# Kernel optimization log

Measured on AMD Instinct MI355X. Metric: run time of the kernel, lower is better.

Reference implementation:

```python
import jax, jax.numpy as jnp
import numpy as np

B, H, S, D = 4, 16, 2048, 128

def setup_inputs() -> dict:
    key = jax.random.key(0)
    kq, kk, kv = jax.random.split(key, 3)
    Q = jax.random.normal(kq, (B, H, S, D), dtype=jnp.float32)
    K = jax.random.normal(kk, (B, H, S, D), dtype=jnp.float32)
    V = jax.random.normal(kv, (B, H, S, D), dtype=jnp.float32)
    # causal mask: True = attend (lower triangle incl. diagonal)
    mask = jnp.tril(jnp.ones((S, S), dtype=jnp.bool_))[None, None, :, :]
    return {"Q": Q, "K": K, "V": V, "mask": mask}

def reference(Q, K, V, mask):
    d_k = Q.shape[-1]
    scale = 1.0 / jnp.sqrt(jnp.asarray(d_k, Q.dtype))
    # [B,H,Sq,Sk] score matrix (naive, materialized, as in the original)
    scores = jnp.einsum('bhqd,bhkd->bhqk', Q, K) * scale
    scores = jnp.where(mask, scores, jnp.asarray(-1e9, scores.dtype))
    attn = jax.nn.softmax(scores, axis=-1)
    return jnp.einsum('bhqk,bhkd->bhqd', attn, V)
```

## Files before the change

kernel.cpp:

```cpp
#include <hip/hip_runtime.h>
#include <hip/hip_bf16.h>

constexpr int S_LEN = 2048;
constexpr int D_DIM = 128;
constexpr int NBH   = 64;
constexpr int NKT   = 32;
constexpr size_t TILE_SHORTS = 64 * 128;
constexpr size_t PAIR_SHORTS = 2 * TILE_SHORTS;
constexpr size_t WS_NEEDED   = (size_t)NBH * NKT * PAIR_SHORTS * 2;

typedef __attribute__((ext_vector_type(8))) short short8;
typedef __attribute__((ext_vector_type(4))) float f32x4;

__device__ __forceinline__ short f2bf(float f) {
    unsigned u = __builtin_bit_cast(unsigned, f);
    u += 0x7fffu + ((u >> 16) & 1u);
    return (short)(u >> 16);
}

__device__ __forceinline__ int kpos(int dc, int key) { return dc ^ (key & 15); }
__device__ __forceinline__ int vpos(int kc, int d) {
    return kc ^ ((d >> 3) & 7) ^ (d & 7);
}

__global__ __launch_bounds__(256)
void preprocess_kv(const float* __restrict__ K, const float* __restrict__ V,
                   short* __restrict__ ws) {
    __shared__ short sv[128 * 64];
    const int tid = threadIdx.x;
    const int kt  = blockIdx.x;
    const int bh  = blockIdx.y;
    const size_t inbase = ((size_t)bh * S_LEN + (size_t)kt * 64) * D_DIM;
    short* wk = ws + ((size_t)bh * NKT + kt) * PAIR_SHORTS;
    short* wv = wk + TILE_SHORTS;

    for (int it = 0; it < 4; ++it) {
        const int idx = (it * 256 + tid) * 8;
        const int key = idx >> 7, d = idx & 127;
        const float* kp = K + inbase + (size_t)key * D_DIM + d;
        float4 a = *reinterpret_cast<const float4*>(kp);
        float4 b = *reinterpret_cast<const float4*>(kp + 4);
        short8 f;
        f[0]=f2bf(a.x); f[1]=f2bf(a.y); f[2]=f2bf(a.z); f[3]=f2bf(a.w);
        f[4]=f2bf(b.x); f[5]=f2bf(b.y); f[6]=f2bf(b.z); f[7]=f2bf(b.w);
        *reinterpret_cast<short8*>(&wk[key * 128 + (kpos(d >> 3, key) << 3)]) = f;
        const float* vp = V + inbase + (size_t)key * D_DIM + d;
        float4 c = *reinterpret_cast<const float4*>(vp);
        float4 e = *reinterpret_cast<const float4*>(vp + 4);
        float vals[8] = {c.x,c.y,c.z,c.w,e.x,e.y,e.z,e.w};
        for (int j = 0; j < 8; ++j) {
            const int dr = d + j;
            sv[dr * 64 + (vpos(key >> 3, dr) << 3) + (key & 7)] = f2bf(vals[j]);
        }
    }
    __syncthreads();
    for (int it = 0; it < 4; ++it) {
        const int off = (it * 256 + tid) * 8;
        *reinterpret_cast<short8*>(&wv[off]) =
            *reinterpret_cast<const short8*>(&sv[off]);
    }
}

__device__ __forceinline__ void async_copy_1k(const short* gsrc, short* ldst,
                                              int lane) {
    __builtin_amdgcn_global_load_lds(
        (const __attribute__((address_space(1))) void*)(gsrc + lane * 8),
        (__attribute__((address_space(3))) void*)ldst, 16, 0, 0);
}

__global__ __launch_bounds__(512, 4)
void fa_causal_main(const float* __restrict__ Q, const short* __restrict__ ws,
                    float* __restrict__ Out) {
    __shared__ short sK[2][64 * 128];
    __shared__ short sVt[128 * 64];
    __shared__ short sP [128 * 64];

    const int tid  = threadIdx.x;
    const int wid  = tid >> 6;
    const int lane = tid & 63;
    const int quad = lane >> 4;
    const int l16  = lane & 15;

    const int k_ = blockIdx.x;
    const int j_ = blockIdx.y;
    const int bh = k_ * 8 + (j_ >> 3);
    const int x  = j_ & 7;

    const size_t base = (size_t)bh * S_LEN * D_DIM;
    const short* tiles = ws + (size_t)bh * NKT * PAIR_SHORTS;
    const float qscale = 0.08838834764831845f * 1.44269504088896340f;

    int nb = 0;
    for (int pi = 0; pi < 2; ++pi) {
        const int qt = (pi == 0) ? (15 - x) : x;
        const int q0 = qt * 128;
        const int kend = 2 * qt + 2;

        for (int i = 0; i < 2; ++i) {
            const int s = wid * 2 + i;
            async_copy_1k(tiles + s * 512, &sK[nb][s * 512], lane);
        }
        short8 vr0, vr1;
        {
            const short* vp = tiles + TILE_SHORTS;
            vr0 = *reinterpret_cast<const short8*>(vp + tid * 8);
            vr1 = *reinterpret_cast<const short8*>(vp + tid * 8 + 4096);
        }

        short8 q_frag[4];
        {
            const float* qp = Q + base + (size_t)(q0 + wid * 16 + l16) * D_DIM;
            for (int kk = 0; kk < 4; ++kk) {
                const int d0 = kk * 32 + quad * 8;
                float4 a = *reinterpret_cast<const float4*>(qp + d0);
                float4 b = *reinterpret_cast<const float4*>(qp + d0 + 4);
                short8 f;
                f[0]=f2bf(a.x*qscale); f[1]=f2bf(a.y*qscale);
                f[2]=f2bf(a.z*qscale); f[3]=f2bf(a.w*qscale);
                f[4]=f2bf(b.x*qscale); f[5]=f2bf(b.y*qscale);
                f[6]=f2bf(b.z*qscale); f[7]=f2bf(b.w*qscale);
                q_frag[kk] = f;
            }
        }

        f32x4 o_acc[8];
        for (int i = 0; i < 8; ++i) o_acc[i] = f32x4{0.f,0.f,0.f,0.f};
        float m_i[4], l_i[4];
        for (int r = 0; r < 4; ++r) { m_i[r] = -1e30f; l_i[r] = 0.f; }

        for (int kt = 0; kt < kend; ++kt) {
            __syncthreads();

            *reinterpret_cast<short8*>(&sVt[tid * 8]) = vr0;
            *reinterpret_cast<short8*>(&sVt[tid * 8 + 4096]) = vr1;

            if (kt + 1 < kend) {
                const short* nk = tiles + (size_t)(kt + 1) * PAIR_SHORTS;
                for (int i = 0; i < 2; ++i) {
                    const int s = wid * 2 + i;
                    async_copy_1k(nk + s * 512, &sK[nb ^ 1][s * 512], lane);
                }
                const short* nv = nk + TILE_SHORTS;
                vr0 = *reinterpret_cast<const short8*>(nv + tid * 8);
                vr1 = *reinterpret_cast<const short8*>(nv + tid * 8 + 4096);
            }

            const int kb    = kt * 64;
            const int wrow0 = q0 + wid * 16;
            const bool active = (kb <= wrow0 + 15);

            f32x4 s_acc[4];
            if (active) {
                __builtin_amdgcn_s_setprio(1);
                for (int ct = 0; ct < 4; ++ct) {
                    const int key = ct * 16 + l16;
                    f32x4 acc = f32x4{0.f,0.f,0.f,0.f};
                    for (int kk = 0; kk < 4; ++kk) {
                        short8 kf = *reinterpret_cast<const short8*>(
                            &sK[nb][key * 128 + (kpos(kk * 4 + quad, key) << 3)]);
                        acc = __builtin_amdgcn_mfma_f32_16x16x32_bf16(q_frag[kk], kf, acc, 0, 0, 0);
                    }
                    s_acc[ct] = acc;
                }
                __builtin_amdgcn_s_setprio(0);

                if (kb + 63 > wrow0) {
                    for (int ct = 0; ct < 4; ++ct) {
                        const int kg = kb + ct * 16 + l16;
                        for (int r = 0; r < 4; ++r)
                            if (kg > wrow0 + quad * 4 + r) s_acc[ct][r] = -1e30f;
                    }
                }

                float tm[4];
                for (int r = 0; r < 4; ++r)
                    tm[r] = fmaxf(fmaxf(s_acc[0][r], s_acc[1][r]),
                                  fmaxf(s_acc[2][r], s_acc[3][r]));
                for (int off = 1; off < 16; off <<= 1)
                    for (int r = 0; r < 4; ++r)
                        tm[r] = fmaxf(tm[r], __shfl_xor(tm[r], off));
                bool grow = false;
                for (int r = 0; r < 4; ++r)
                    grow = grow || (tm[r] - m_i[r] > 8.0f);
                if (__any(grow)) {
                    for (int r = 0; r < 4; ++r) {
                        const float mn = fmaxf(m_i[r], tm[r]);
                        const float a  = __builtin_amdgcn_exp2f(m_i[r] - mn);
                        m_i[r] = mn;
                        l_i[r] *= a;
                        for (int nt = 0; nt < 8; ++nt) o_acc[nt][r] *= a;
                    }
                }
                float rs[4] = {0.f, 0.f, 0.f, 0.f};
                for (int ct = 0; ct < 4; ++ct)
                    for (int r = 0; r < 4; ++r) {
                        const float p = __builtin_amdgcn_exp2f(s_acc[ct][r] - m_i[r]);
                        s_acc[ct][r] = p;
                        rs[r] += p;
                    }
                for (int off = 1; off < 16; off <<= 1)
                    for (int r = 0; r < 4; ++r)
                        rs[r] += __shfl_xor(rs[r], off);
                for (int r = 0; r < 4; ++r) l_i[r] += rs[r];

                for (int ct = 0; ct < 4; ++ct)
                    for (int r = 0; r < 4; ++r) {
                        const int row = wid * 16 + quad * 4 + r;
                        const int col = ct * 16 + l16;
                        sP[row * 64 + (((col >> 3) ^ (row & 7)) << 3) + (col & 7)]
                            = f2bf(s_acc[ct][r]);
                    }
            }

            asm volatile("s_waitcnt lgkmcnt(0)" ::: "memory");
            __builtin_amdgcn_s_barrier();
            asm volatile("" ::: "memory");

            if (active) {
                const int prow = wid * 16 + l16;
                short8 pf[2];
                for (int k2 = 0; k2 < 2; ++k2)
                    pf[k2] = *reinterpret_cast<const short8*>(
                        &sP[prow * 64 + (((k2 * 4 + quad) ^ (prow & 7)) << 3)]);
                __builtin_amdgcn_s_setprio(1);
                for (int nt = 0; nt < 8; ++nt) {
                    const int vrow = nt * 16 + l16;
                    for (int k2 = 0; k2 < 2; ++k2) {
                        short8 vf = *reinterpret_cast<const short8*>(
                            &sVt[vrow * 64 + (vpos(k2 * 4 + quad, vrow) << 3)]);
                        o_acc[nt] = __builtin_amdgcn_mfma_f32_16x16x32_bf16(pf[k2], vf, o_acc[nt], 0, 0, 0);
                    }
                }
                __builtin_amdgcn_s_setprio(0);
            }
            nb ^= 1;
        }

        for (int r = 0; r < 4; ++r) {
            const float inv = 1.0f / l_i[r];
            const int qrow = q0 + wid * 16 + quad * 4 + r;
            float* op = Out + base + (size_t)qrow * D_DIM;
            for (int nt = 0; nt < 8; ++nt)
                op[nt * 16 + l16] = o_acc[nt][r] * inv;
        }
    }
}

constexpr int SK_STRIDE  = 136;
constexpr int SVT_STRIDE = 72;
constexpr int SP_STRIDE  = 72;

__global__ __launch_bounds__(256, 4)
void fa_causal_fallback(const float* __restrict__ Q, const float* __restrict__ K,
                        const float* __restrict__ V, float* __restrict__ Out) {
    __shared__ short sK[64 * SK_STRIDE];
    __shared__ short sVt[128 * SVT_STRIDE];
    short* sP = sK;
    const int tid  = threadIdx.x;
    const int wid  = tid >> 6;
    const int lane = tid & 63;
    const int quad = lane >> 4;
    const int l16  = lane & 15;
    const int x  = blockIdx.x;
    const int bh = blockIdx.y;
    const size_t base = (size_t)bh * S_LEN * D_DIM;
    const float scale = 0.08838834764831845f;
    for (int pi = 0; pi < 2; ++pi) {
        const int qt = (pi == 0) ? (31 - x) : x;
        const int q0 = qt * 64;
        short8 q_frag[4];
        {
            const float* qp = Q + base + (size_t)(q0 + wid * 16 + l16) * D_DIM;
            for (int kk = 0; kk < 4; ++kk) {
                const int d0 = kk * 32 + quad * 8;
                float4 a = *reinterpret_cast<const float4*>(qp + d0);
                float4 b = *reinterpret_cast<const float4*>(qp + d0 + 4);
                short8 f;
                f[0]=f2bf(a.x*scale); f[1]=f2bf(a.y*scale);
                f[2]=f2bf(a.z*scale); f[3]=f2bf(a.w*scale);
                f[4]=f2bf(b.x*scale); f[5]=f2bf(b.y*scale);
                f[6]=f2bf(b.z*scale); f[7]=f2bf(b.w*scale);
                q_frag[kk] = f;
            }
        }
        f32x4 o_acc[8];
        for (int i = 0; i < 8; ++i) o_acc[i] = f32x4{0.f,0.f,0.f,0.f};
        float m_i[4], l_i[4];
        for (int r = 0; r < 4; ++r) { m_i[r] = -1e30f; l_i[r] = 0.f; }
        for (int kt = 0; kt <= qt; ++kt) {
            for (int it = 0; it < 4; ++it) {
                const int idx = (it * 256 + tid) * 8;
                const int key = idx >> 7, d = idx & 127;
                const float* kp = K + base + (size_t)(kt * 64 + key) * D_DIM + d;
                float4 a = *reinterpret_cast<const float4*>(kp);
                float4 b = *reinterpret_cast<const float4*>(kp + 4);
                short8 f;
                f[0]=f2bf(a.x); f[1]=f2bf(a.y); f[2]=f2bf(a.z); f[3]=f2bf(a.w);
                f[4]=f2bf(b.x); f[5]=f2bf(b.y); f[6]=f2bf(b.z); f[7]=f2bf(b.w);
                *reinterpret_cast<short8*>(&sK[key * SK_STRIDE + d]) = f;
            }
            for (int it = 0; it < 4; ++it) {
                const int idx = (it * 256 + tid) * 8;
                const int key = idx >> 7, d = idx & 127;
                const int kc = key >> 3, kw = key & 7;
                const float* vp = V + base + (size_t)(kt * 64 + key) * D_DIM + d;
                float4 a = *reinterpret_cast<const float4*>(vp);
                float4 b = *reinterpret_cast<const float4*>(vp + 4);
                float vals[8] = {a.x,a.y,a.z,a.w,b.x,b.y,b.z,b.w};
                const int rc = (d >> 3) & 7;
                const int cs = (kc ^ rc) * 8 + kw;
                for (int j = 0; j < 8; ++j)
                    sVt[(d + j) * SVT_STRIDE + cs] = f2bf(vals[j]);
            }
            __syncthreads();
            f32x4 s_acc[4];
            for (int ct = 0; ct < 4; ++ct) {
                f32x4 acc = f32x4{0.f,0.f,0.f,0.f};
                for (int kk = 0; kk < 4; ++kk) {
                    short8 kf = *reinterpret_cast<const short8*>(
                        &sK[(ct * 16 + l16) * SK_STRIDE + kk * 32 + quad * 8]);
                    acc = __builtin_amdgcn_mfma_f32_16x16x32_bf16(q_frag[kk], kf, acc, 0, 0, 0);
                }
                s_acc[ct] = acc;
            }
            if (kt == qt) {
                for (int ct = 0; ct < 4; ++ct) {
                    const int kg = ct * 16 + l16;
                    for (int r = 0; r < 4; ++r)
                        if (kg > wid * 16 + quad * 4 + r) s_acc[ct][r] = -1e30f;
                }
            }
            float tm[4];
            for (int r = 0; r < 4; ++r)
                tm[r] = fmaxf(fmaxf(s_acc[0][r], s_acc[1][r]),
                              fmaxf(s_acc[2][r], s_acc[3][r]));
            for (int off = 1; off < 16; off <<= 1)
                for (int r = 0; r < 4; ++r)
                    tm[r] = fmaxf(tm[r], __shfl_xor(tm[r], off));
            float alpha[4], m_new[4], rs[4];
            for (int r = 0; r < 4; ++r) {
                m_new[r] = fmaxf(m_i[r], tm[r]);
                alpha[r] = __expf(m_i[r] - m_new[r]);
                rs[r] = 0.f;
            }
            for (int ct = 0; ct < 4; ++ct)
                for (int r = 0; r < 4; ++r) {
                    float p = __expf(s_acc[ct][r] - m_new[r]);
                    s_acc[ct][r] = p;
                    rs[r] += p;
                }
            for (int off = 1; off < 16; off <<= 1)
                for (int r = 0; r < 4; ++r)
                    rs[r] += __shfl_xor(rs[r], off);
            for (int r = 0; r < 4; ++r) {
                l_i[r] = alpha[r] * l_i[r] + rs[r];
                m_i[r] = m_new[r];
            }
            for (int nt = 0; nt < 8; ++nt)
                for (int r = 0; r < 4; ++r)
                    o_acc[nt][r] *= alpha[r];
            __syncthreads();
            for (int ct = 0; ct < 4; ++ct)
                for (int r = 0; r < 4; ++r) {
                    const int row = wid * 16 + quad * 4 + r;
                    const int col = ct * 16 + l16;
                    sP[row * SP_STRIDE + (((col >> 3) ^ ((row >> 2) & 7)) << 3) + (col & 7)]
                        = f2bf(s_acc[ct][r]);
                }
            {
                const int prow = wid * 16 + l16;
                const int pxr  = (prow >> 2) & 7;
                for (int nt = 0; nt < 8; ++nt) {
                    const int vrow = nt * 16 + l16;
                    const int vxr  = (vrow >> 3) & 7;
                    for (int k2 = 0; k2 < 2; ++k2) {
                        const int chunk = k2 * 4 + quad;
                        short8 pf = *reinterpret_cast<const short8*>(
                            &sP[prow * SP_STRIDE + ((chunk ^ pxr) << 3)]);
                        short8 vf = *reinterpret_cast<const short8*>(
                            &sVt[vrow * SVT_STRIDE + ((chunk ^ vxr) << 3)]);
                        o_acc[nt] = __builtin_amdgcn_mfma_f32_16x16x32_bf16(pf, vf, o_acc[nt], 0, 0, 0);
                    }
                }
            }
            __syncthreads();
        }
        for (int nt = 0; nt < 8; ++nt)
            for (int r = 0; r < 4; ++r) {
                const int qrow = q0 + wid * 16 + quad * 4 + r;
                Out[base + (size_t)qrow * D_DIM + nt * 16 + l16] = o_acc[nt][r] / l_i[r];
            }
    }
}

extern "C" void kernel_launch(void* const* d_in, const int* in_sizes, int n_in,
                              void* d_out, int out_size, void* d_ws, size_t ws_size,
                              hipStream_t stream) {
    const float* Q = (const float*)d_in[0];
    const float* K = (const float*)d_in[1];
    const float* V = (const float*)d_in[2];
    float* Out = (float*)d_out;

    if (ws_size >= WS_NEEDED) {
        short* ws = (short*)d_ws;
        preprocess_kv<<<dim3(NKT, NBH), 256, 0, stream>>>(K, V, ws);
        fa_causal_main<<<dim3(8, NBH), 512, 0, stream>>>(Q, ws, Out);
    } else {
        fa_causal_fallback<<<dim3(16, NBH), 256, 0, stream>>>(Q, K, V, Out);
    }
}
```

Measured before the change: 465.8 us.

## Shrink causal attention blocks to 64-row Q tiles with single-buffered K

Each main-kernel block now owns 64 query rows and runs 4 warps (256 threads) instead of 128 rows and 8 warps. The grid doubles, and a flattened block index is remapped so that batch-head pairs are interleaved. The K tile becomes single-buffered: the next K/V prefetch is issued after the score barrier, and the P-tile store moves after that barrier. Per-warp inactive-tile checks disappear because every warp in a 64-row tile covers the same key range. The aim is to cut causal idle work and LDS footprint and to raise occupancy, at the cost of less K reuse per block and less overlap between loads and compute.

```diff
diff --git a/kernel.cpp b/kernel.cpp
--- a/kernel.cpp
+++ b/kernel.cpp
@@ -68,12 +68,12 @@
         (__attribute__((address_space(3))) void*)ldst, 16, 0, 0);
 }
 
-__global__ __launch_bounds__(512, 4)
+__global__ __launch_bounds__(256, 4)
 void fa_causal_main(const float* __restrict__ Q, const short* __restrict__ ws,
                     float* __restrict__ Out) {
-    __shared__ short sK[2][64 * 128];
+    __shared__ short sK [64 * 128];
     __shared__ short sVt[128 * 64];
-    __shared__ short sP [128 * 64];
+    __shared__ short sP [64 * 64];
 
     const int tid  = threadIdx.x;
     const int wid  = tid >> 6;
@@ -81,30 +81,27 @@
     const int quad = lane >> 4;
     const int l16  = lane & 15;
 
-    const int k_ = blockIdx.x;
-    const int j_ = blockIdx.y;
-    const int bh = k_ * 8 + (j_ >> 3);
-    const int x  = j_ & 7;
+    const int flat = blockIdx.x + (blockIdx.y << 4);
+    const int bh   = ((flat & 7) << 3) | ((flat >> 3) & 7);
+    const int x    = flat >> 6;
 
     const size_t base = (size_t)bh * S_LEN * D_DIM;
     const short* tiles = ws + (size_t)bh * NKT * PAIR_SHORTS;
     const float qscale = 0.08838834764831845f * 1.44269504088896340f;
 
-    int nb = 0;
     for (int pi = 0; pi < 2; ++pi) {
-        const int qt = (pi == 0) ? (15 - x) : x;
-        const int q0 = qt * 128;
-        const int kend = 2 * qt + 2;
-
-        for (int i = 0; i < 2; ++i) {
-            const int s = wid * 2 + i;
-            async_copy_1k(tiles + s * 512, &sK[nb][s * 512], lane);
-        }
-        short8 vr0, vr1;
+        const int qt = (pi == 0) ? (31 - x) : x;
+        const int q0 = qt * 64;
+
+        for (int i = 0; i < 4; ++i) {
+            const int s = wid * 4 + i;
+            async_copy_1k(tiles + s * 512, &sK[s * 512], lane);
+        }
+        short8 vr[4];
         {
             const short* vp = tiles + TILE_SHORTS;
-            vr0 = *reinterpret_cast<const short8*>(vp + tid * 8);
-            vr1 = *reinterpret_cast<const short8*>(vp + tid * 8 + 4096);
+            for (int i = 0; i < 4; ++i)
+                vr[i] = *reinterpret_cast<const short8*>(vp + (i * 256 + tid) * 8);
         }
 
         short8 q_frag[4];
@@ -128,95 +125,89 @@
         float m_i[4], l_i[4];
         for (int r = 0; r < 4; ++r) { m_i[r] = -1e30f; l_i[r] = 0.f; }
 
-        for (int kt = 0; kt < kend; ++kt) {
+        for (int kt = 0; kt <= qt; ++kt) {
             __syncthreads();
 
-            *reinterpret_cast<short8*>(&sVt[tid * 8]) = vr0;
-            *reinterpret_cast<short8*>(&sVt[tid * 8 + 4096]) = vr1;
-
-            if (kt + 1 < kend) {
-                const short* nk = tiles + (size_t)(kt + 1) * PAIR_SHORTS;
-                for (int i = 0; i < 2; ++i) {
-                    const int s = wid * 2 + i;
-                    async_copy_1k(nk + s * 512, &sK[nb ^ 1][s * 512], lane);
-                }
-                const short* nv = nk + TILE_SHORTS;
-                vr0 = *reinterpret_cast<const short8*>(nv + tid * 8);
-                vr1 = *reinterpret_cast<const short8*>(nv + tid * 8 + 4096);
-            }
-
-            const int kb    = kt * 64;
-            const int wrow0 = q0 + wid * 16;
-            const bool active = (kb <= wrow0 + 15);
+            for (int i = 0; i < 4; ++i)
+                *reinterpret_cast<short8*>(&sVt[(i * 256 + tid) * 8]) = vr[i];
 
             f32x4 s_acc[4];
-            if (active) {
-                __builtin_amdgcn_s_setprio(1);
+            __builtin_amdgcn_s_setprio(1);
+            for (int ct = 0; ct < 4; ++ct) {
+                const int key = ct * 16 + l16;
+                f32x4 acc = f32x4{0.f,0.f,0.f,0.f};
+                for (int kk = 0; kk < 4; ++kk) {
+                    short8 kf = *reinterpret_cast<const short8*>(
+                        &sK[key * 128 + (kpos(kk * 4 + quad, key) << 3)]);
+                    acc = __builtin_amdgcn_mfma_f32_16x16x32_bf16(q_frag[kk], kf, acc, 0, 0, 0);
+                }
+                s_acc[ct] = acc;
+            }
+            __builtin_amdgcn_s_setprio(0);
+
+            if (kt == qt) {
                 for (int ct = 0; ct < 4; ++ct) {
-                    const int key = ct * 16 + l16;
-                    f32x4 acc = f32x4{0.f,0.f,0.f,0.f};
-                    for (int kk = 0; kk < 4; ++kk) {
-                        short8 kf = *reinterpret_cast<const short8*>(
-                            &sK[nb][key * 128 + (kpos(kk * 4 + quad, key) << 3)]);
-                        acc = __builtin_amdgcn_mfma_f32_16x16x32_bf16(q_frag[kk], kf, acc, 0, 0, 0);
-                    }
-                    s_acc[ct] = acc;
-                }
-                __builtin_amdgcn_s_setprio(0);
-
-                if (kb + 63 > wrow0) {
-                    for (int ct = 0; ct < 4; ++ct) {
-                        const int kg = kb + ct * 16 + l16;
-                        for (int r = 0; r < 4; ++r)
-                            if (kg > wrow0 + quad * 4 + r) s_acc[ct][r] = -1e30f;
-                    }
-                }
-
-                float tm[4];
+                    const int kg = ct * 16 + l16;
+                    for (int r = 0; r < 4; ++r)
+                        if (kg > wid * 16 + quad * 4 + r) s_acc[ct][r] = -1e30f;
+                }
+            }
+
+            float tm[4];
+            for (int r = 0; r < 4; ++r)
+                tm[r] = fmaxf(fmaxf(s_acc[0][r], s_acc[1][r]),
+                              fmaxf(s_acc[2][r], s_acc[3][r]));
+            for (int off = 1; off < 16; off <<= 1)
                 for (int r = 0; r < 4; ++r)
-                    tm[r] = fmaxf(fmaxf(s_acc[0][r], s_acc[1][r]),
-                                  fmaxf(s_acc[2][r], s_acc[3][r]));
-                for (int off = 1; off < 16; off <<= 1)
-                    for (int r = 0; r < 4; ++r)
-                        tm[r] = fmaxf(tm[r], __shfl_xor(tm[r], off));
-                bool grow = false;
+                    tm[r] = fmaxf(tm[r], __shfl_xor(tm[r], off));
+            bool grow = false;
+            for (int r = 0; r < 4; ++r)
+                grow = grow || (tm[r] - m_i[r] > 8.0f);
+            if (__any(grow)) {
+                for (int r = 0; r < 4; ++r) {
+                    const float mn = fmaxf(m_i[r], tm[r]);
+                    const float a  = __builtin_amdgcn_exp2f(m_i[r] - mn);
+                    m_i[r] = mn;
+                    l_i[r] *= a;
+                    for (int nt = 0; nt < 8; ++nt) o_acc[nt][r] *= a;
+                }
+            }
+            float rs[4] = {0.f, 0.f, 0.f, 0.f};
+            for (int ct = 0; ct < 4; ++ct)
+                for (int r = 0; r < 4; ++r) {
+                    const float p = __builtin_amdgcn_exp2f(s_acc[ct][r] - m_i[r]);
+                    s_acc[ct][r] = p;
+                    rs[r] += p;
+                }
+            for (int off = 1; off < 16; off <<= 1)
                 for (int r = 0; r < 4; ++r)
-                    grow = grow || (tm[r] - m_i[r] > 8.0f);
-                if (__any(grow)) {
-                    for (int r = 0; r < 4; ++r) {
-                        const float mn = fmaxf(m_i[r], tm[r]);
-                        const float a  = __builtin_amdgcn_exp2f(m_i[r] - mn);
-                        m_i[r] = mn;
-                        l_i[r] *= a;
-                        for (int nt = 0; nt < 8; ++nt) o_acc[nt][r] *= a;
-                    }
-                }
-                float rs[4] = {0.f, 0.f, 0.f, 0.f};
-                for (int ct = 0; ct < 4; ++ct)
-                    for (int r = 0; r < 4; ++r) {
-                        const float p = __builtin_amdgcn_exp2f(s_acc[ct][r] - m_i[r]);
-                        s_acc[ct][r] = p;
-                        rs[r] += p;
-                    }
-                for (int off = 1; off < 16; off <<= 1)
-                    for (int r = 0; r < 4; ++r)
-                        rs[r] += __shfl_xor(rs[r], off);
-                for (int r = 0; r < 4; ++r) l_i[r] += rs[r];
-
-                for (int ct = 0; ct < 4; ++ct)
-                    for (int r = 0; r < 4; ++r) {
-                        const int row = wid * 16 + quad * 4 + r;
-                        const int col = ct * 16 + l16;
-                        sP[row * 64 + (((col >> 3) ^ (row & 7)) << 3) + (col & 7)]
-                            = f2bf(s_acc[ct][r]);
-                    }
-            }
+                    rs[r] += __shfl_xor(rs[r], off);
+            for (int r = 0; r < 4; ++r) l_i[r] += rs[r];
 
             asm volatile("s_waitcnt lgkmcnt(0)" ::: "memory");
             __builtin_amdgcn_s_barrier();
             asm volatile("" ::: "memory");
 
-            if (active) {
+            if (kt < qt) {
+                const short* nk = tiles + (size_t)(kt + 1) * PAIR_SHORTS;
+                for (int i = 0; i < 4; ++i) {
+                    const int s = wid * 4 + i;
+                    async_copy_1k(nk + s * 512, &sK[s * 512], lane);
+                }
+                const short* nv = nk + TILE_SHORTS;
+                for (int i = 0; i < 4; ++i)
+                    vr[i] = *reinterpret_cast<const short8*>(nv + (i * 256 + tid) * 8);
+            }
+
+            for (int ct = 0; ct < 4; ++ct)
+                for (int r = 0; r < 4; ++r) {
+                    const int row = wid * 16 + quad * 4 + r;
+                    const int col = ct * 16 + l16;
+                    sP[row * 64 + (((col >> 3) ^ (row & 7)) << 3) + (col & 7)]
+                        = f2bf(s_acc[ct][r]);
+                }
+
+            {
                 const int prow = wid * 16 + l16;
                 short8 pf[2];
                 for (int k2 = 0; k2 < 2; ++k2)
@@ -233,7 +224,6 @@
                 }
                 __builtin_amdgcn_s_setprio(0);
             }
-            nb ^= 1;
         }
 
         for (int r = 0; r < 4; ++r) {
@@ -404,7 +394,7 @@
     if (ws_size >= WS_NEEDED) {
         short* ws = (short*)d_ws;
         preprocess_kv<<<dim3(NKT, NBH), 256, 0, stream>>>(K, V, ws);
-        fa_causal_main<<<dim3(8, NBH), 512, 0, stream>>>(Q, ws, Out);
+        fa_causal_main<<<dim3(16, NBH), 256, 0, stream>>>(Q, ws, Out);
     } else {
         fa_causal_fallback<<<dim3(16, NBH), 256, 0, stream>>>(Q, K, V, Out);
     }
```

Result: slower. 532.6 us (+14.4%).
